# Kernel tuning notes

Measured on AMD Instinct MI355X. Metric: run time of the kernel, lower is better.

The kernel has to match this reference:

```python
import jax, jax.numpy as jnp
import numpy as np

B, L, D = 4, 4096, 128
BLOCK, SPARSITY = 64, 0.9
NEG = -1e9


def _make_block_mask(key):
    nb = L // BLOCK
    bm = jax.random.uniform(key, (nb, nb)) > SPARSITY
    bm = bm | jnp.eye(nb, dtype=bool)  # keep diagonal blocks so no row is fully masked
    bm = jnp.tril(bm)
    return jnp.repeat(jnp.repeat(bm, BLOCK, axis=0), BLOCK, axis=1)  # [L, L]


def _xavier(key, shape):
    limit = float(np.sqrt(6.0 / (shape[0] + shape[1])))
    return jax.random.uniform(key, shape, jnp.float32, -limit, limit)


def setup_inputs() -> dict:
    key = jax.random.key(0)
    ks = jax.random.split(key, 10)
    t = lambda k: jax.random.normal(k, (B, L, D), jnp.float32)
    return {
        'q_real': t(ks[0]), 'q_imag': t(ks[1]),
        'k_real': t(ks[2]), 'k_imag': t(ks[3]),
        'v_real': t(ks[4]), 'v_imag': t(ks[5]),
        'W_qkv': _xavier(ks[6], (6 * D, 6 * D)),
        'b_qkv': jnp.zeros((6 * D,), jnp.float32),
        'W_out': _xavier(ks[7], (2 * D, 2 * D)),
        'b_out': jnp.zeros((2 * D,), jnp.float32),
        'block_mask': _make_block_mask(ks[8]),
    }


def reference(q_real, q_imag, k_real, k_imag, v_real, v_imag,
              W_qkv, b_qkv, W_out, b_out, block_mask):
    d = q_real.shape[-1]
    scale = d ** -0.5
    # fused qkv projection over the 6 concatenated channels
    x = jnp.concatenate([q_real, q_imag, k_real, k_imag, v_real, v_imag], axis=-1)  # [B,L,6D]
    qkv = (x @ W_qkv.T + b_qkv).reshape(x.shape[0], x.shape[1], 6, d)
    q_r, q_i, k_r, k_i, v_r, v_i = (qkv[:, :, j] for j in range(6))

    def attn(q, k, v):
        s = jnp.einsum('bqd,bkd->bqk', q, k) * scale          # [B,L,L]
        s = jnp.where(block_mask[None], s, NEG)               # block-sparse mask
        a = jax.nn.softmax(s, axis=-1)                        # dropout = identity (eval)
        return jnp.einsum('bqk,bkd->bqd', a, v)

    out = jnp.concatenate([attn(q_r, k_r, v_r), attn(q_i, k_i, v_i)], axis=-1)  # [B,L,2D]
    out = out @ W_out.T + b_out
    return out[..., :d], out[..., d:]
```

## Files before the change

kernel.cpp:

```cpp
#include <hip/hip_runtime.h>
#include <hip/hip_bf16.h>

typedef unsigned short u16;
typedef __attribute__((ext_vector_type(8))) short bf16x8;
typedef __attribute__((ext_vector_type(4))) float f32x4;

#define SEQ_L 4096
#define M_TOT 16384

__device__ __forceinline__ float bf2f(u16 x) {
    unsigned u = ((unsigned)x) << 16;
    return __builtin_bit_cast(float, u);
}
__device__ __forceinline__ u16 f2bf(float f) {
    unsigned u = __builtin_bit_cast(unsigned, f);
    u += 0x7FFFu + ((u >> 16) & 1u);
    return (u16)(u >> 16);
}
__device__ __forceinline__ unsigned cvt_pk_bf16(float lo, float hi) {
    unsigned r;
    asm("v_cvt_pk_bf16_f32 %0, %1, %2" : "=v"(r) : "v"(lo), "v"(hi));
    return r;
}
__device__ __forceinline__ void gload16(const u16* g, u16* l) {
    __builtin_amdgcn_global_load_lds(
        (const __attribute__((address_space(1))) unsigned int*)g,
        (__attribute__((address_space(3))) unsigned int*)l, 16, 0, 0);
}

__global__ __launch_bounds__(256) void prep_all(
    const float* __restrict__ in0, const float* __restrict__ in1, const float* __restrict__ in2,
    const float* __restrict__ in3, const float* __restrict__ in4, const float* __restrict__ in5,
    const float* __restrict__ Wqkv, const float* __restrict__ Wout, const void* __restrict__ mask,
    u16* __restrict__ x, u16* __restrict__ Wqkv_bf, u16* __restrict__ Wout_bf,
    unsigned long long* __restrict__ bmap) {
    int id = blockIdx.x * 256 + threadIdx.x;
    if (id < 1572864) {
        const float* ins[6] = {in0, in1, in2, in3, in4, in5};
        int which = id >> 18, j = id & 262143;
        int m = j >> 4, c8 = j & 15;
        const float* sp = ins[which] + (size_t)m * 128 + c8 * 8;
        float4 a = *(const float4*)sp;
        float4 b = *(const float4*)(sp + 4);
        u16 t[8] = {f2bf(a.x), f2bf(a.y), f2bf(a.z), f2bf(a.w),
                    f2bf(b.x), f2bf(b.y), f2bf(b.z), f2bf(b.w)};
        *(uint4*)(x + (size_t)m * 768 + which * 128 + c8 * 8) = *(uint4*)t;
    } else if (id < 1572864 + 73728 + 8192) {
        int i = id - 1572864;
        const float* src = (i < 73728) ? Wqkv : Wout;
        u16* dst = (i < 73728) ? Wqkv_bf : Wout_bf;
        if (i >= 73728) i -= 73728;
        const float* sp = src + (size_t)i * 8;
        float4 a = *(const float4*)sp;
        float4 b = *(const float4*)(sp + 4);
        u16 t[8] = {f2bf(a.x), f2bf(a.y), f2bf(a.z), f2bf(a.w),
                    f2bf(b.x), f2bf(b.y), f2bf(b.z), f2bf(b.w)};
        *(uint4*)(dst + (size_t)i * 8) = *(uint4*)t;
    } else if (id < 1572864 + 73728 + 8192 + 4096) {
        int i = id - 1572864 - 73728 - 8192;
        int bi = i >> 6, bj = i & 63;
        size_t e = (size_t)(bi * 64) * SEQ_L + (size_t)bj * 64;
        const unsigned char* p8 = (const unsigned char*)mask;
        unsigned w0 = *(const unsigned*)mask;
        bool v;
        if (w0 == 0x01010101u || w0 == 0xFFFFFFFFu)      v = p8[e] != 0;
        else if (w0 == 0x3F803F80u || w0 == 0x3C003C00u) v = ((const u16*)mask)[e] != 0;
        else                                             v = ((const unsigned*)mask)[e] != 0;
        unsigned long long bits = __ballot(v);
        if ((i & 63) == 0) bmap[bi] = bits;
    }
}

__global__ __launch_bounds__(256, 3) void qkv_gemm(
    const u16* __restrict__ X, const u16* __restrict__ W, const float* __restrict__ bias,
    u16* __restrict__ qk, u16* __restrict__ vt) {
    __shared__ __align__(16) u16 As[128 * 64];
    __shared__ __align__(16) u16 Bs[128 * 64];
    int m0 = blockIdx.x * 128, n0 = blockIdx.y * 128;
    int tid = threadIdx.x, lane = tid & 63, w = tid >> 6;
    int ln = lane & 15, quad = lane >> 4;
    int rw = (w >> 1) * 64, cw = (w & 1) * 64;
    int lr8 = lane >> 3, lc = lane & 7;
    f32x4 acc[4][4] = {};
    for (int kk = 0; kk < 768; kk += 64) {
        __syncthreads();
        #pragma unroll
        for (int j = 0; j < 4; j++) {
            int r0 = w * 32 + j * 8, r = r0 + lr8;
            gload16(X + (size_t)(m0 + r) * 768 + kk + ((lc ^ (r & 7)) * 8), As + r0 * 64 + lane * 8);
            gload16(W + (size_t)(n0 + r) * 768 + kk + ((lc ^ (r & 7)) * 8), Bs + r0 * 64 + lane * 8);
        }
        __syncthreads();
        #pragma unroll
        for (int s = 0; s < 2; s++) {
            bf16x8 af[4], bfr[4];
            #pragma unroll
            for (int i = 0; i < 4; i++) {
                int R = rw + i * 16 + ln;
                af[i] = *(const bf16x8*)(As + R * 64 + ((4 * s + quad) ^ (ln & 7)) * 8);
            }
            #pragma unroll
            for (int t = 0; t < 4; t++) {
                int R = cw + t * 16 + ln;
                bfr[t] = *(const bf16x8*)(Bs + R * 64 + ((4 * s + quad) ^ (ln & 7)) * 8);
            }
            #pragma unroll
            for (int i = 0; i < 4; i++)
                #pragma unroll
                for (int t = 0; t < 4; t++)
                    acc[i][t] = __builtin_amdgcn_mfma_f32_16x16x32_bf16(af[i], bfr[t], acc[i][t], 0, 0, 0);
        }
    }
    if (n0 < 512) {
        #pragma unroll
        for (int i = 0; i < 4; i++) {
            int row0 = m0 + rw + i * 16 + 4 * quad;
            #pragma unroll
            for (int t = 0; t < 4; t++) {
                int col = n0 + cw + t * 16 + ln;
                float bv = bias[col];
                #pragma unroll
                for (int r = 0; r < 4; r++)
                    qk[(size_t)(row0 + r) * 512 + col] = f2bf(acc[i][t][r] + bv);
            }
        }
    } else {
        #pragma unroll
        for (int i = 0; i < 4; i++) {
            int row0 = m0 + rw + i * 16 + 4 * quad;
            int b = row0 >> 12, seq = row0 & 4095;
            #pragma unroll
            for (int t = 0; t < 4; t++) {
                int col = n0 + cw + t * 16 + ln;
                float bv = bias[col];
                int d = col - 512;
                u16 pk[4] = {f2bf(acc[i][t][0] + bv), f2bf(acc[i][t][1] + bv),
                             f2bf(acc[i][t][2] + bv), f2bf(acc[i][t][3] + bv)};
                *(ushort4*)(vt + ((size_t)(b * 2 + (d >> 7)) * 128 + (d & 127)) * SEQ_L + seq)
                    = *(ushort4*)pk;
            }
        }
    }
}

__global__ __launch_bounds__(256, 2) void attn_sparse(
    const u16* __restrict__ qk, const u16* __restrict__ vt,
    const unsigned long long* __restrict__ bmap, u16* __restrict__ attn_bf) {
    __shared__ __align__(16) u16 Ks[2][64 * 128];
    __shared__ __align__(16) u16 Vs[2][128 * 64];

    int lane = threadIdx.x & 63, w = threadIdx.x >> 6;
    int ln = lane & 15, quad = lane >> 4;
    int u = blockIdx.x >> 3, v = blockIdx.x & 7;
    int qi = (u < 32) ? (63 - u) : (u - 32);
    int b = v >> 1, ch = v & 1;
    int rowbase = b * SEQ_L + qi * 64 + w * 16;
    const float scale = 0.08838834764831845f;

    bf16x8 qf[4];
    {
        const u16* qp = qk + (size_t)(rowbase + ln) * 512 + ch * 128;
        #pragma unroll
        for (int s = 0; s < 4; s++) qf[s] = *(const bf16x8*)(qp + 32 * s + 8 * quad);
    }

    float m_st = -1e30f, l_st = 0.f;
    f32x4 accO[8] = {};

    const u16* kbase0 = qk + (size_t)b * SEQ_L * 512 + 256 + ch * 128;
    const u16* vbase0 = vt + (size_t)(b * 2 + ch) * 128 * SEQ_L;
    unsigned long long bm = bmap[qi];

    int kb = __ffsll(bm) - 1; bm &= bm - 1;
    {
        const u16* kp = kbase0 + (size_t)(kb * 64) * 512;
        const u16* vp = vbase0 + kb * 64;
        #pragma unroll
        for (int j = 0; j < 4; j++) {
            int kr = w * 16 + j * 4 + (lane >> 4);
            gload16(kp + (size_t)kr * 512 + (((lane & 15) ^ (kr & 7)) * 8),
                    Ks[0] + (w * 16 + j * 4) * 128 + lane * 8);
        }
        #pragma unroll
        for (int j = 0; j < 4; j++) {
            int d = w * 32 + j * 8 + (lane >> 3);
            gload16(vp + (size_t)d * SEQ_L + (((lane & 7) ^ (d & 7)) * 8),
                    Vs[0] + (w * 32 + j * 8) * 64 + lane * 8);
        }
    }

    int srcA = ln + ((quad & 1) << 5);
    int srcB = srcA + 16;
    bool hi = (quad & 2) != 0;

    int bufc = 0;
    while (true) {
        int nkb = -1;
        if (bm) {
            nkb = __ffsll(bm) - 1; bm &= bm - 1;
            const u16* kp = kbase0 + (size_t)(nkb * 64) * 512;
            const u16* vp = vbase0 + nkb * 64;
            u16* Kd = Ks[bufc ^ 1];
            u16* Vd = Vs[bufc ^ 1];
            #pragma unroll
            for (int j = 0; j < 4; j++) {
                int kr = w * 16 + j * 4 + (lane >> 4);
                gload16(kp + (size_t)kr * 512 + (((lane & 15) ^ (kr & 7)) * 8),
                        Kd + (w * 16 + j * 4) * 128 + lane * 8);
            }
            #pragma unroll
            for (int j = 0; j < 4; j++) {
                int d = w * 32 + j * 8 + (lane >> 3);
                gload16(vp + (size_t)d * SEQ_L + (((lane & 7) ^ (d & 7)) * 8),
                        Vd + (w * 32 + j * 8) * 64 + lane * 8);
            }
        }
        if (nkb >= 0) __builtin_amdgcn_s_waitcnt(0x0F78);
        else          __builtin_amdgcn_s_waitcnt(0x0F70);
        __builtin_amdgcn_s_barrier();

        const u16* K = Ks[bufc];
        const u16* V = Vs[bufc];

        f32x4 accS[4] = {};
        #pragma unroll
        for (int s = 0; s < 4; s++)
            #pragma unroll
            for (int t = 0; t < 4; t++) {
                bf16x8 kf = *(const bf16x8*)(K + (t * 16 + ln) * 128 +
                                             (((4 * s + quad) ^ (ln & 7)) * 8));
                accS[t] = __builtin_amdgcn_mfma_f32_16x16x32_bf16(kf, qf[s], accS[t], 0, 0, 0);
            }

        float mx = fmaxf(fmaxf(fmaxf(accS[0][0], accS[0][1]), fmaxf(accS[0][2], accS[0][3])),
                         fmaxf(fmaxf(fmaxf(accS[1][0], accS[1][1]), fmaxf(accS[1][2], accS[1][3])),
                               fmaxf(fmaxf(fmaxf(accS[2][0], accS[2][1]), fmaxf(accS[2][2], accS[2][3])),
                                     fmaxf(fmaxf(accS[3][0], accS[3][1]), fmaxf(accS[3][2], accS[3][3])))));
        mx = fmaxf(mx, __shfl_xor(mx, 16, 64));
        mx = fmaxf(mx, __shfl_xor(mx, 32, 64));
        float nm = fmaxf(m_st, mx * scale);
        float alpha = __expf(m_st - nm);
        m_st = nm;

        float p[4][4];
        float rs = 0.f;
        #pragma unroll
        for (int t = 0; t < 4; t++)
            #pragma unroll
            for (int r = 0; r < 4; r++) {
                p[t][r] = __expf(accS[t][r] * scale - nm);
                rs += p[t][r];
            }
        rs += __shfl_xor(rs, 16, 64);
        rs += __shfl_xor(rs, 32, 64);
        l_st = l_st * alpha + rs;

        unsigned uA[4], uB[4];
        #pragma unroll
        for (int t = 0; t < 4; t++) {
            uA[t] = cvt_pk_bf16(p[t][0], p[t][1]);
            uB[t] = cvt_pk_bf16(p[t][2], p[t][3]);
        }

        float al[4];
        #pragma unroll
        for (int r = 0; r < 4; r++) al[r] = __shfl(alpha, 4 * quad + r, 64);
        #pragma unroll
        for (int nt = 0; nt < 8; nt++)
            #pragma unroll
            for (int r = 0; r < 4; r++) accO[nt][r] *= al[r];

        #pragma unroll
        for (int h = 0; h < 2; h++) {
            unsigned a0 = (unsigned)__shfl((int)uA[2 * h], srcA, 64);
            unsigned a1 = (unsigned)__shfl((int)uA[2 * h + 1], srcA, 64);
            unsigned b0 = (unsigned)__shfl((int)uB[2 * h], srcA, 64);
            unsigned b1 = (unsigned)__shfl((int)uB[2 * h + 1], srcA, 64);
            unsigned c0 = (unsigned)__shfl((int)uA[2 * h], srcB, 64);
            unsigned c1 = (unsigned)__shfl((int)uA[2 * h + 1], srcB, 64);
            unsigned d0 = (unsigned)__shfl((int)uB[2 * h], srcB, 64);
            unsigned d1 = (unsigned)__shfl((int)uB[2 * h + 1], srcB, 64);
            union { unsigned w4[4]; bf16x8 v; } pu;
            pu.w4[0] = hi ? a1 : a0;
            pu.w4[1] = hi ? b1 : b0;
            pu.w4[2] = hi ? c1 : c0;
            pu.w4[3] = hi ? d1 : d0;
            bf16x8 pf = pu.v;
            #pragma unroll
            for (int nt = 0; nt < 8; nt++) {
                bf16x8 vf = *(const bf16x8*)(V + (nt * 16 + ln) * 64 +
                                             (((4 * h + quad) ^ (ln & 7)) * 8));
                accO[nt] = __builtin_amdgcn_mfma_f32_16x16x32_bf16(pf, vf, accO[nt], 0, 0, 0);
            }
        }

        if (nkb < 0) break;
        __builtin_amdgcn_s_barrier();
        bufc ^= 1;
    }

    float linv = 1.0f / fmaxf(l_st, 1e-20f);
    float inv[4];
    #pragma unroll
    for (int r = 0; r < 4; r++) inv[r] = __shfl(linv, 4 * quad + r, 64);
    #pragma unroll
    for (int nt = 0; nt < 8; nt++)
        #pragma unroll
        for (int r = 0; r < 4; r++)
            attn_bf[(size_t)(rowbase + 4 * quad + r) * 256 + ch * 128 + nt * 16 + ln]
                = f2bf(accO[nt][r] * inv[r]);
}

__global__ __launch_bounds__(256, 3) void out_gemm(
    const u16* __restrict__ A, const u16* __restrict__ W, const float* __restrict__ bias,
    float* __restrict__ out) {
    __shared__ __align__(16) u16 As[128 * 64];
    __shared__ __align__(16) u16 Bs[128 * 64];
    int m0 = blockIdx.x * 128, n0 = blockIdx.y * 128;
    int tid = threadIdx.x, lane = tid & 63, w = tid >> 6;
    int ln = lane & 15, quad = lane >> 4;
    int rw = (w >> 1) * 64, cw = (w & 1) * 64;
    int lr8 = lane >> 3, lc = lane & 7;
    f32x4 acc[4][4] = {};
    for (int kk = 0; kk < 256; kk += 64) {
        __syncthreads();
        #pragma unroll
        for (int j = 0; j < 4; j++) {
            int r0 = w * 32 + j * 8, r = r0 + lr8;
            gload16(A + (size_t)(m0 + r) * 256 + kk + ((lc ^ (r & 7)) * 8), As + r0 * 64 + lane * 8);
            gload16(W + (size_t)(n0 + r) * 256 + kk + ((lc ^ (r & 7)) * 8), Bs + r0 * 64 + lane * 8);
        }
        __syncthreads();
        #pragma unroll
        for (int s = 0; s < 2; s++) {
            bf16x8 af[4], bfr[4];
            #pragma unroll
            for (int i = 0; i < 4; i++) {
                int R = rw + i * 16 + ln;
                af[i] = *(const bf16x8*)(As + R * 64 + ((4 * s + quad) ^ (ln & 7)) * 8);
            }
            #pragma unroll
            for (int t = 0; t < 4; t++) {
                int R = cw + t * 16 + ln;
                bfr[t] = *(const bf16x8*)(Bs + R * 64 + ((4 * s + quad) ^ (ln & 7)) * 8);
            }
            #pragma unroll
            for (int i = 0; i < 4; i++)
                #pragma unroll
                for (int t = 0; t < 4; t++)
                    acc[i][t] = __builtin_amdgcn_mfma_f32_16x16x32_bf16(af[i], bfr[t], acc[i][t], 0, 0, 0);
        }
    }
    const size_t half = (size_t)M_TOT * 128;
    #pragma unroll
    for (int i = 0; i < 4; i++) {
        int row0 = m0 + rw + i * 16 + 4 * quad;
        #pragma unroll
        for (int t = 0; t < 4; t++) {
            int col = n0 + cw + t * 16 + ln;
            float bv = bias[col];
            float* base = (col < 128) ? (out + col) : (out + half + (col - 128));
            #pragma unroll
            for (int r = 0; r < 4; r++)
                base[(size_t)(row0 + r) * 128] = acc[i][t][r] + bv;
        }
    }
}

extern "C" void kernel_launch(void* const* d_in, const int* in_sizes, int n_in,
                              void* d_out, int out_size, void* d_ws, size_t ws_size,
                              hipStream_t stream) {
    char* ws = (char*)d_ws;
    u16* x_bf    = (u16*)ws;
    u16* qk_buf  = x_bf + (size_t)M_TOT * 768;
    u16* vt_buf  = qk_buf + (size_t)M_TOT * 512;
    u16* attn_bf = vt_buf + (size_t)1024 * SEQ_L;
    u16* Wqkv_bf = attn_bf + (size_t)M_TOT * 256;
    u16* Wout_bf = Wqkv_bf + 589824;
    unsigned long long* bmap = (unsigned long long*)(Wout_bf + 65536);

    hipLaunchKernelGGL(prep_all, dim3(6480), dim3(256), 0, stream,
                       (const float*)d_in[0], (const float*)d_in[1], (const float*)d_in[2],
                       (const float*)d_in[3], (const float*)d_in[4], (const float*)d_in[5],
                       (const float*)d_in[6], (const float*)d_in[8], d_in[10],
                       x_bf, Wqkv_bf, Wout_bf, bmap);
    hipLaunchKernelGGL(qkv_gemm, dim3(128, 6), dim3(256), 0, stream,
                       x_bf, Wqkv_bf, (const float*)d_in[7], qk_buf, vt_buf);
    hipLaunchKernelGGL(attn_sparse, dim3(512), dim3(256), 0, stream,
                       qk_buf, vt_buf, bmap, attn_bf);
    hipLaunchKernelGGL(out_gemm, dim3(128, 2), dim3(256), 0, stream,
                       attn_bf, Wout_bf, (const float*)d_in[9], (float*)d_out);
}
```

Measured before the change: 197.3 us.

## Enlarge QKV GEMM tiles to 256x256 with double-buffered LDS prefetch

```diff
diff --git a/kernel.cpp b/kernel.cpp
--- a/kernel.cpp
+++ b/kernel.cpp
@@ -71,71 +71,106 @@
     }
 }
 
-__global__ __launch_bounds__(256, 3) void qkv_gemm(
+__global__ __launch_bounds__(512, 2) void qkv_gemm(
     const u16* __restrict__ X, const u16* __restrict__ W, const float* __restrict__ bias,
     u16* __restrict__ qk, u16* __restrict__ vt) {
-    __shared__ __align__(16) u16 As[128 * 64];
-    __shared__ __align__(16) u16 Bs[128 * 64];
-    int m0 = blockIdx.x * 128, n0 = blockIdx.y * 128;
+    __shared__ __align__(16) u16 Al[2][256 * 64];
+    __shared__ __align__(16) u16 Bl[2][256 * 64];
+    int m0 = blockIdx.x * 256, n0 = blockIdx.y * 256;
     int tid = threadIdx.x, lane = tid & 63, w = tid >> 6;
+    int wr = w >> 2, wc = w & 3;
     int ln = lane & 15, quad = lane >> 4;
-    int rw = (w >> 1) * 64, cw = (w & 1) * 64;
     int lr8 = lane >> 3, lc = lane & 7;
-    f32x4 acc[4][4] = {};
-    for (int kk = 0; kk < 768; kk += 64) {
-        __syncthreads();
-        #pragma unroll
-        for (int j = 0; j < 4; j++) {
-            int r0 = w * 32 + j * 8, r = r0 + lr8;
-            gload16(X + (size_t)(m0 + r) * 768 + kk + ((lc ^ (r & 7)) * 8), As + r0 * 64 + lane * 8);
-            gload16(W + (size_t)(n0 + r) * 768 + kk + ((lc ^ (r & 7)) * 8), Bs + r0 * 64 + lane * 8);
-        }
-        __syncthreads();
-        #pragma unroll
-        for (int s = 0; s < 2; s++) {
-            bf16x8 af[4], bfr[4];
-            #pragma unroll
-            for (int i = 0; i < 4; i++) {
-                int R = rw + i * 16 + ln;
-                af[i] = *(const bf16x8*)(As + R * 64 + ((4 * s + quad) ^ (ln & 7)) * 8);
-            }
-            #pragma unroll
-            for (int t = 0; t < 4; t++) {
-                int R = cw + t * 16 + ln;
-                bfr[t] = *(const bf16x8*)(Bs + R * 64 + ((4 * s + quad) ^ (ln & 7)) * 8);
-            }
-            #pragma unroll
-            for (int i = 0; i < 4; i++)
+    f32x4 acc[8][4] = {};
+
+    #pragma unroll
+    for (int j = 0; j < 4; j++) {
+        int r = j * 64 + w * 8 + lr8;
+        gload16(X + (size_t)(m0 + r) * 768 + ((lc ^ (r & 7)) * 8),
+                Al[0] + (j * 64 + w * 8) * 64 + lane * 8);
+        gload16(W + (size_t)(n0 + r) * 768 + ((lc ^ (r & 7)) * 8),
+                Bl[0] + (j * 64 + w * 8) * 64 + lane * 8);
+    }
+
+    for (int T = 0; T < 12; T++) {
+        int pi = T & 1;
+        __builtin_amdgcn_s_waitcnt(0x0F70);
+        __builtin_amdgcn_s_barrier();
+        __builtin_amdgcn_sched_barrier(0);
+        if (T + 1 < 12) {
+            int kk = (T + 1) * 64;
+            #pragma unroll
+            for (int j = 0; j < 4; j++) {
+                int r = j * 64 + w * 8 + lr8;
+                gload16(X + (size_t)(m0 + r) * 768 + kk + ((lc ^ (r & 7)) * 8),
+                        Al[pi ^ 1] + (j * 64 + w * 8) * 64 + lane * 8);
+                gload16(W + (size_t)(n0 + r) * 768 + kk + ((lc ^ (r & 7)) * 8),
+                        Bl[pi ^ 1] + (j * 64 + w * 8) * 64 + lane * 8);
+            }
+        }
+        const u16* A = Al[pi];
+        const u16* B = Bl[pi];
+        __builtin_amdgcn_s_setprio(1);
+        #pragma unroll
+        for (int mh = 0; mh < 2; mh++)
+            #pragma unroll
+            for (int nh = 0; nh < 2; nh++) {
+                bf16x8 af[4][2], bfr[2][2];
                 #pragma unroll
-                for (int t = 0; t < 4; t++)
-                    acc[i][t] = __builtin_amdgcn_mfma_f32_16x16x32_bf16(af[i], bfr[t], acc[i][t], 0, 0, 0);
-        }
-    }
+                for (int mi = 0; mi < 4; mi++)
+                    #pragma unroll
+                    for (int ks = 0; ks < 2; ks++) {
+                        int R = wr * 128 + mh * 64 + mi * 16 + ln;
+                        af[mi][ks] = *(const bf16x8*)(A + R * 64 +
+                                       (((4 * ks + quad) ^ (ln & 7)) * 8));
+                    }
+                #pragma unroll
+                for (int ni = 0; ni < 2; ni++)
+                    #pragma unroll
+                    for (int ks = 0; ks < 2; ks++) {
+                        int R = wc * 64 + nh * 32 + ni * 16 + ln;
+                        bfr[ni][ks] = *(const bf16x8*)(B + R * 64 +
+                                        (((4 * ks + quad) ^ (ln & 7)) * 8));
+                    }
+                #pragma unroll
+                for (int mi = 0; mi < 4; mi++)
+                    #pragma unroll
+                    for (int ni = 0; ni < 2; ni++)
+                        #pragma unroll
+                        for (int ks = 0; ks < 2; ks++)
+                            acc[mh * 4 + mi][nh * 2 + ni] =
+                                __builtin_amdgcn_mfma_f32_16x16x32_bf16(
+                                    af[mi][ks], bfr[ni][ks],
+                                    acc[mh * 4 + mi][nh * 2 + ni], 0, 0, 0);
+            }
+        __builtin_amdgcn_s_setprio(0);
+    }
+
     if (n0 < 512) {
         #pragma unroll
-        for (int i = 0; i < 4; i++) {
-            int row0 = m0 + rw + i * 16 + 4 * quad;
-            #pragma unroll
-            for (int t = 0; t < 4; t++) {
-                int col = n0 + cw + t * 16 + ln;
+        for (int mi8 = 0; mi8 < 8; mi8++) {
+            int row0 = m0 + wr * 128 + mi8 * 16 + 4 * quad;
+            #pragma unroll
+            for (int ni4 = 0; ni4 < 4; ni4++) {
+                int col = n0 + wc * 64 + ni4 * 16 + ln;
                 float bv = bias[col];
                 #pragma unroll
                 for (int r = 0; r < 4; r++)
-                    qk[(size_t)(row0 + r) * 512 + col] = f2bf(acc[i][t][r] + bv);
+                    qk[(size_t)(row0 + r) * 512 + col] = f2bf(acc[mi8][ni4][r] + bv);
             }
         }
     } else {
         #pragma unroll
-        for (int i = 0; i < 4; i++) {
-            int row0 = m0 + rw + i * 16 + 4 * quad;
+        for (int mi8 = 0; mi8 < 8; mi8++) {
+            int row0 = m0 + wr * 128 + mi8 * 16 + 4 * quad;
             int b = row0 >> 12, seq = row0 & 4095;
             #pragma unroll
-            for (int t = 0; t < 4; t++) {
-                int col = n0 + cw + t * 16 + ln;
+            for (int ni4 = 0; ni4 < 4; ni4++) {
+                int col = n0 + wc * 64 + ni4 * 16 + ln;
                 float bv = bias[col];
                 int d = col - 512;
-                u16 pk[4] = {f2bf(acc[i][t][0] + bv), f2bf(acc[i][t][1] + bv),
-                             f2bf(acc[i][t][2] + bv), f2bf(acc[i][t][3] + bv)};
+                u16 pk[4] = {f2bf(acc[mi8][ni4][0] + bv), f2bf(acc[mi8][ni4][1] + bv),
+                             f2bf(acc[mi8][ni4][2] + bv), f2bf(acc[mi8][ni4][3] + bv)};
                 *(ushort4*)(vt + ((size_t)(b * 2 + (d >> 7)) * 128 + (d & 127)) * SEQ_L + seq)
                     = *(ushort4*)pk;
             }
@@ -384,7 +419,7 @@
                        (const float*)d_in[3], (const float*)d_in[4], (const float*)d_in[5],
                        (const float*)d_in[6], (const float*)d_in[8], d_in[10],
                        x_bf, Wqkv_bf, Wout_bf, bmap);
-    hipLaunchKernelGGL(qkv_gemm, dim3(128, 6), dim3(256), 0, stream,
+    hipLaunchKernelGGL(qkv_gemm, dim3(64, 3), dim3(512), 0, stream,
                        x_bf, Wqkv_bf, (const float*)d_in[7], qk_buf, vt_buf);
     hipLaunchKernelGGL(attn_sparse, dim3(512), dim3(256), 0, stream,
                        qk_buf, vt_buf, bmap, attn_bf);
```

Result: slower. 204.3 us (+3.5%).
